# Optimization experiments

Measured on AMD Instinct MI355X. Metric: run time of the kernel, lower is better.

## Reference

```python
import jax, jax.numpy as jnp
import numpy as np

N_HEAD = 12
SEQ = 4096
D_MODEL = 768


def setup_inputs() -> dict:
    key = jax.random.key(0)
    ks = jax.random.split(key, 5)
    tokens = jax.random.normal(ks[0], (SEQ, D_MODEL), dtype=jnp.float32)
    # GPT-2 causal mask buffer: lower-triangular ones, shape [1,1,n_ctx,n_ctx]
    attn_bias = jnp.tril(jnp.ones((SEQ, SEQ), dtype=jnp.float32))[None, None]
    c_attn_weight = jax.random.normal(ks[1], (D_MODEL, 3 * D_MODEL), dtype=jnp.float32) * 0.02
    c_attn_bias = jax.random.normal(ks[2], (3 * D_MODEL,), dtype=jnp.float32) * 0.02
    c_proj_weight = jax.random.normal(ks[3], (D_MODEL, D_MODEL), dtype=jnp.float32) * 0.02
    c_proj_bias = jax.random.normal(ks[4], (D_MODEL,), dtype=jnp.float32) * 0.02
    return {
        "tokens": tokens,
        "attn_bias": attn_bias,
        "c_attn_weight": c_attn_weight,
        "c_attn_bias": c_attn_bias,
        "c_proj_weight": c_proj_weight,
        "c_proj_bias": c_proj_bias,
    }


def reference(tokens, attn_bias, c_attn_weight, c_attn_bias, c_proj_weight, c_proj_bias):
    S, D = tokens.shape
    H = N_HEAD
    hd = D // H
    qkv = tokens @ c_attn_weight + c_attn_bias          # [S, 3D]
    q, k, v = jnp.split(qkv, 3, axis=1)                 # each [S, D]
    q = q.reshape(S, H, hd).transpose(1, 0, 2)          # [H, S, hd]
    kh = k.reshape(S, H, hd).transpose(1, 2, 0)         # [H, hd, S] (key pre-transposed)
    vh = v.reshape(S, H, hd).transpose(1, 0, 2)         # [H, S, hd]
    w = jnp.einsum('hqd,hdk->hqk', q, kh) / jnp.sqrt(jnp.float32(hd))  # [H, S, S]
    nd, ns = S, S
    b = attn_bias[0, :, ns - nd:ns, :ns]                # [1, S, S], broadcasts over heads
    w = w * b - 1e10 * (1.0 - b)
    p = jax.nn.softmax(w, axis=-1)
    a = jnp.einsum('hqk,hkd->hqd', p, vh)               # [H, S, hd]
    a = a.transpose(1, 0, 2).reshape(S, D)              # merge heads
    out = a @ c_proj_weight + c_proj_bias               # [S, D]
    return out
```

## Files before the change

kernel.cpp:

```cpp
#include <hip/hip_runtime.h>

typedef __attribute__((ext_vector_type(8))) short s8v;
typedef __attribute__((ext_vector_type(2))) float f32x2;
typedef __attribute__((ext_vector_type(4))) float f32x4;
typedef __attribute__((ext_vector_type(16))) float f32x16;
typedef __attribute__((ext_vector_type(4))) unsigned short u16x4;
typedef __attribute__((ext_vector_type(4))) unsigned int u32x4;
typedef __attribute__((ext_vector_type(4))) _Float16 h16x4;

#define SEQ 4096
#define DM  768
#define NH  12
#define HD  64
#define QSCL 0.18033688f
#define FOFF 8.0f

__device__ __forceinline__ unsigned short f2bf(float f) {
  union { float f; unsigned int u; } v; v.f = f;
  unsigned int r = v.u + 0x7fffu + ((v.u >> 16) & 1u);
  return (unsigned short)(r >> 16);
}

__device__ __forceinline__ unsigned int cvtpk(float lo, float hi) {
  unsigned int r;
  asm("v_cvt_pk_bf16_f32 %0, %1, %2" : "=v"(r) : "v"(lo), "v"(hi));
  return r;
}

__device__ __forceinline__ void gload16(const void* g, void* l) {
  __builtin_amdgcn_global_load_lds((const __attribute__((address_space(1))) void*)g,
                                   (__attribute__((address_space(3))) void*)l, 16, 0, 0);
}

__global__ __launch_bounds__(256) void k_prep(
    const float* __restrict__ tokens, const float* __restrict__ wqkv,
    const float* __restrict__ wproj, unsigned short* __restrict__ tok,
    unsigned short* __restrict__ wqkvT, unsigned short* __restrict__ wprojT) {
  __shared__ float tile[32][33];
  const int b = blockIdx.x;
  const int tid = threadIdx.x;
  if (b < 3072) {
    int i = (b * 256 + tid) * 4;
    float4 v = *reinterpret_cast<const float4*>(tokens + i);
    u16x4 o;
    o.x = f2bf(v.x); o.y = f2bf(v.y); o.z = f2bf(v.z); o.w = f2bf(v.w);
    *reinterpret_cast<u16x4*>(tok + i) = o;
    return;
  }
  const float* in;
  unsigned short* out;
  int idx, N;
  if (b < 4800) { idx = b - 3072; in = wqkv;  out = wqkvT;  N = 2304; }
  else          { idx = b - 4800; in = wproj; out = wprojT; N = 768;  }
  const int k0 = (idx % 24) * 32, n0 = (idx / 24) * 32;
  const int tr = tid >> 5, tc = tid & 31;
#pragma unroll
  for (int i = 0; i < 4; i++)
    tile[i * 8 + tr][tc] = in[(k0 + i * 8 + tr) * N + n0 + tc];
  __syncthreads();
#pragma unroll
  for (int i = 0; i < 4; i++)
    out[(n0 + i * 8 + tr) * 768 + k0 + tc] = f2bf(tile[tc][i * 8 + tr]);
}

template<int MODE>
__global__ __launch_bounds__(256) void k_gemm(
    const unsigned short* __restrict__ A, const unsigned short* __restrict__ BT,
    const float* __restrict__ bias,
    unsigned short* __restrict__ Oq, unsigned short* __restrict__ Ok,
    unsigned short* __restrict__ Ov, float* __restrict__ Of) {
  __shared__ unsigned short As[128 * 32];
  __shared__ unsigned short Bs[128 * 32];
  const int tid = threadIdx.x;
  const int lane = tid & 63;
  const int w = tid >> 6;
  const int wm = w >> 1, wn = w & 1;
  const int l15 = lane & 15, l4 = lane >> 4;
  const int m0 = blockIdx.x * 128, n0 = blockIdx.y * 128;

  f32x4 acc[4][4] = {};

  int srow[2], skc[2];
#pragma unroll
  for (int j = 0; j < 2; j++) {
    int slot = j * 256 + tid;
    srow[j] = slot >> 2;
    skc[j] = (slot & 3) ^ ((srow[j] >> 1) & 3);
  }
  const int ldsb0 = (tid & ~63) * 16;
  const int ldsb1 = (256 + (tid & ~63)) * 16;

  for (int k0 = 0; k0 < DM; k0 += 32) {
    gload16(A + (m0 + srow[0]) * DM + k0 + skc[0] * 8, (char*)As + ldsb0);
    gload16(A + (m0 + srow[1]) * DM + k0 + skc[1] * 8, (char*)As + ldsb1);
    gload16(BT + (n0 + srow[0]) * DM + k0 + skc[0] * 8, (char*)Bs + ldsb0);
    gload16(BT + (n0 + srow[1]) * DM + k0 + skc[1] * 8, (char*)Bs + ldsb1);
    __syncthreads();
    s8v af[4], bfr[4];
#pragma unroll
    for (int i = 0; i < 4; i++) {
      int ra = wm * 64 + i * 16 + l15;
      int ca = (l4 ^ ((ra >> 1) & 3)) * 8;
      af[i] = *reinterpret_cast<const s8v*>(&As[ra * 32 + ca]);
      int rb = wn * 64 + i * 16 + l15;
      int cb = (l4 ^ ((rb >> 1) & 3)) * 8;
      bfr[i] = *reinterpret_cast<const s8v*>(&Bs[rb * 32 + cb]);
    }
#pragma unroll
    for (int mi = 0; mi < 4; mi++)
#pragma unroll
      for (int nj = 0; nj < 4; nj++)
        acc[mi][nj] = __builtin_amdgcn_mfma_f32_16x16x32_bf16(af[mi], bfr[nj], acc[mi][nj], 0, 0, 0);
    __syncthreads();
  }

#pragma unroll
  for (int nj = 0; nj < 4; nj++) {
    const int col = n0 + wn * 64 + nj * 16 + l15;
    const float bv = bias[col];
#pragma unroll
    for (int mi = 0; mi < 4; mi++) {
      const int rowb = m0 + wm * 64 + mi * 16 + l4 * 4;
      if (MODE == 0) {
        if (col < 768) {
#pragma unroll
          for (int r = 0; r < 4; r++)
            Oq[(rowb + r) * DM + col] = f2bf((acc[mi][nj][r] + bv) * QSCL);
        } else if (col < 1536) {
#pragma unroll
          for (int r = 0; r < 4; r++)
            Ok[(rowb + r) * DM + (col - 768)] = f2bf(acc[mi][nj][r] + bv);
        } else {
          u16x4 pk;
#pragma unroll
          for (int r = 0; r < 4; r++)
            pk[r] = f2bf(acc[mi][nj][r] + bv);
          *reinterpret_cast<u16x4*>(&Ov[(col - 1536) * SEQ + rowb]) = pk;
        }
      } else {
#pragma unroll
        for (int r = 0; r < 4; r++)
          Of[(rowb + r) * DM + col] = acc[mi][nj][r] + bv;
      }
    }
  }
}

__global__ __launch_bounds__(256, 4) void k_attn(
    const unsigned short* __restrict__ Qb, const unsigned short* __restrict__ Kb,
    const unsigned short* __restrict__ Vt, _Float16* __restrict__ Opart,
    float* __restrict__ lw) {
  __shared__ unsigned short Ks[2][64 * 64];
  __shared__ unsigned short Vs[2][64 * 64];
  const int tid = threadIdx.x;
  const int lane = tid & 63;
  const int w = tid >> 6;
  const int l31 = lane & 31, lh = lane >> 5;
  const int bid = blockIdx.x;
  const int s = bid & 3;
  const int b2 = bid >> 2;
  const int head = b2 % NH;
  const int qt = 31 - (b2 / NH);
  const int q0w = qt * 128 + w * 32;
  const int ntiles = 2 * qt + 2;

  const unsigned short* const Kh = Kb + head * HD;
  const unsigned short* const Vh = Vt + head * HD * SEQ;

  int srow[2], scol[2];
#pragma unroll
  for (int j = 0; j < 2; j++) {
    int c = j * 256 + tid;
    srow[j] = c >> 3;
    scol[j] = ((c & 7) ^ (srow[j] & 7)) * 8;
  }
  const int ldsoff0 = (tid & ~63) * 16;
  const int ldsoff1 = 4096 + (tid & ~63) * 16;
  int koff0 = (s * 64 + srow[0]) * DM + scol[0];
  int koff1 = (s * 64 + srow[1]) * DM + scol[1];
  int voff0 = srow[0] * SEQ + s * 64 + scol[0];
  int voff1 = srow[1] * SEQ + s * 64 + scol[1];

  s8v aq[4];
#pragma unroll
  for (int kc = 0; kc < 4; kc++)
    aq[kc] = *reinterpret_cast<const s8v*>(
        &Qb[(q0w + l31) * DM + head * HD + kc * 16 + lh * 8]);

  const int x7 = l31 & 7;
  const int rbase = l31 * 128;

  f32x16 O0 = {}, O1 = {};
  float lsum = 0.f;

  if (s < ntiles) {
    gload16(Kh + koff0, (char*)Ks[0] + ldsoff0);
    gload16(Kh + koff1, (char*)Ks[0] + ldsoff1);
    gload16(Vh + voff0, (char*)Vs[0] + ldsoff0);
    gload16(Vh + voff1, (char*)Vs[0] + ldsoff1);
    __asm__ volatile("s_waitcnt vmcnt(0)" ::: "memory");
  }
  __syncthreads();
  koff0 += 256 * DM; koff1 += 256 * DM;
  voff0 += 256;      voff1 += 256;

  for (int t = s; t < ntiles; t += 4) {
    const int cur = ((t - s) >> 2) & 1;
    if (t + 4 < ntiles) {
      const int nxt = cur ^ 1;
      gload16(Kh + koff0, (char*)Ks[nxt] + ldsoff0);
      gload16(Kh + koff1, (char*)Ks[nxt] + ldsoff1);
      gload16(Vh + voff0, (char*)Vs[nxt] + ldsoff0);
      gload16(Vh + voff1, (char*)Vs[nxt] + ldsoff1);
    }
    koff0 += 256 * DM; koff1 += 256 * DM;
    voff0 += 256;      voff1 += 256;
    const int kb = t * 64;
    if (kb <= q0w + 31) {
      const char* const kbuf = (const char*)Ks[cur];
      const char* const vbuf = (const char*)Vs[cur];
      f32x16 z0, z1;
#pragma unroll
      for (int r = 0; r < 16; r++) { z0[r] = -FOFF; z1[r] = -FOFF; }
      __builtin_amdgcn_s_setprio(1);
#pragma unroll
      for (int kc = 0; kc < 4; kc++) {
        const int so = ((kc * 2 + lh) ^ x7) << 4;
        const s8v k0 = *reinterpret_cast<const s8v*>(kbuf + rbase + so);
        const s8v k1 = *reinterpret_cast<const s8v*>(kbuf + 4096 + rbase + so);
        z0 = __builtin_amdgcn_mfma_f32_32x32x16_bf16(k0, aq[kc], z0, 0, 0, 0);
        z1 = __builtin_amdgcn_mfma_f32_32x32x16_bf16(k1, aq[kc], z1, 0, 0, 0);
      }
      __builtin_amdgcn_s_setprio(0);
      if (kb + 63 > q0w) {
        const int qm = q0w + l31 - kb - 4 * lh;
#pragma unroll
        for (int r = 0; r < 16; r++) {
          const int koff = (r & 3) + 8 * (r >> 2);
          z0[r] = (koff > qm) ? -1e30f : z0[r];
          z1[r] = (koff + 32 > qm) ? -1e30f : z1[r];
        }
      }
      f32x2 sa = {0.f, 0.f}, sb = {0.f, 0.f};
#pragma unroll
      for (int r = 0; r < 8; r++) {
        z0[2 * r] = exp2f(z0[2 * r]);
        z0[2 * r + 1] = exp2f(z0[2 * r + 1]);
        f32x2 e0; e0[0] = z0[2 * r]; e0[1] = z0[2 * r + 1];
        sa += e0;
        z1[2 * r] = exp2f(z1[2 * r]);
        z1[2 * r + 1] = exp2f(z1[2 * r + 1]);
        f32x2 e1; e1[0] = z1[2 * r]; e1[1] = z1[2 * r + 1];
        sb += e1;
      }
      sa += sb;
      lsum += sa[0] + sa[1];
      s8v pf[4];
#define PACKKC(V, base, dst)                                                 \
      {                                                                      \
        unsigned int A0 = cvtpk(V[base + 0], V[base + 1]);                   \
        unsigned int B0 = cvtpk(V[base + 2], V[base + 3]);                   \
        unsigned int A1 = cvtpk(V[base + 4], V[base + 5]);                   \
        unsigned int B1 = cvtpk(V[base + 6], V[base + 7]);                   \
        asm("v_permlane32_swap_b32 %0, %1" : "+v"(A0), "+v"(A1));            \
        asm("v_permlane32_swap_b32 %0, %1" : "+v"(B0), "+v"(B1));            \
        u32x4 q_ = {A0, B0, A1, B1};                                         \
        dst = __builtin_bit_cast(s8v, q_);                                   \
      }
      PACKKC(z0, 0, pf[0]);
      PACKKC(z0, 8, pf[1]);
      PACKKC(z1, 0, pf[2]);
      PACKKC(z1, 8, pf[3]);
#undef PACKKC
      __builtin_amdgcn_s_setprio(1);
#pragma unroll
      for (int kc = 0; kc < 4; kc++) {
        const int so = ((kc * 2 + lh) ^ x7) << 4;
        const s8v v0 = *reinterpret_cast<const s8v*>(vbuf + rbase + so);
        const s8v v1 = *reinterpret_cast<const s8v*>(vbuf + 4096 + rbase + so);
        O0 = __builtin_amdgcn_mfma_f32_32x32x16_bf16(v0, pf[kc], O0, 0, 0, 0);
        O1 = __builtin_amdgcn_mfma_f32_32x32x16_bf16(v1, pf[kc], O1, 0, 0, 0);
      }
      __builtin_amdgcn_s_setprio(0);
    }
    __asm__ volatile("s_waitcnt vmcnt(0)" ::: "memory");
    __syncthreads();
  }

  lsum += __shfl_xor(lsum, 32);
  _Float16* const op = Opart + (size_t)s * SEQ * DM + (size_t)(q0w + l31) * DM +
                       head * HD + 4 * lh;
#pragma unroll
  for (int k = 0; k < 4; k++) {
    h16x4 o0h, o1h;
#pragma unroll
    for (int r = 0; r < 4; r++) {
      o0h[r] = (_Float16)O0[k * 4 + r];
      o1h[r] = (_Float16)O1[k * 4 + r];
    }
    *reinterpret_cast<h16x4*>(op + 8 * k) = o0h;
    *reinterpret_cast<h16x4*>(op + 32 + 8 * k) = o1h;
  }
  if (lh == 0)
    lw[(s * NH + head) * SEQ + q0w + l31] = lsum;
}

__global__ __launch_bounds__(256) void k_merge(const _Float16* __restrict__ Opart,
                                               const float* __restrict__ lw,
                                               unsigned short* __restrict__ attn) {
  const int idx = blockIdx.x * 256 + threadIdx.x;
  const int e4 = idx * 4;
  const int row = e4 / DM;
  const int col = e4 - row * DM;
  const int head = col >> 6;
  const float l0 = lw[(0 * NH + head) * SEQ + row];
  const float l1 = lw[(1 * NH + head) * SEQ + row];
  const float l2 = lw[(2 * NH + head) * SEQ + row];
  const float l3 = lw[(3 * NH + head) * SEQ + row];
  const float rl = 1.f / (l0 + l1 + l2 + l3);
  const size_t SD = (size_t)SEQ * DM;
  const h16x4 o0 = *reinterpret_cast<const h16x4*>(Opart + e4);
  const h16x4 o1 = *reinterpret_cast<const h16x4*>(Opart + SD + e4);
  const h16x4 o2 = *reinterpret_cast<const h16x4*>(Opart + 2 * SD + e4);
  const h16x4 o3 = *reinterpret_cast<const h16x4*>(Opart + 3 * SD + e4);
  u16x4 pk;
#pragma unroll
  for (int j = 0; j < 4; j++)
    pk[j] = f2bf(((float)o0[j] + (float)o1[j] + (float)o2[j] + (float)o3[j]) * rl);
  *reinterpret_cast<u16x4*>(attn + e4) = pk;
}

extern "C" void kernel_launch(void* const* d_in, const int* in_sizes, int n_in,
                              void* d_out, int out_size, void* d_ws, size_t ws_size,
                              hipStream_t stream) {
  (void)in_sizes; (void)n_in; (void)out_size; (void)ws_size;
  const float* tokens = (const float*)d_in[0];
  const float* wqkv  = (const float*)d_in[2];
  const float* bqkv  = (const float*)d_in[3];
  const float* wproj = (const float*)d_in[4];
  const float* bproj = (const float*)d_in[5];
  float* out = (float*)d_out;

  unsigned short* tok    = (unsigned short*)d_ws;
  unsigned short* wqkvT  = tok + 4096 * 768;
  unsigned short* wprojT = wqkvT + 2304 * 768;
  unsigned short* Qb     = wprojT + 768 * 768;
  unsigned short* Kb     = Qb + 4096 * 768;
  unsigned short* Vt     = Kb + 4096 * 768;
  unsigned short* attn   = Vt + 768 * 4096;
  _Float16* Opart = (_Float16*)(attn + 4096 * 768);
  float* lw = (float*)(Opart + 4 * 4096 * 768);

  k_prep<<<5376, 256, 0, stream>>>(tokens, wqkv, wproj, tok, wqkvT, wprojT);
  k_gemm<0><<<dim3(32, 18), 256, 0, stream>>>(tok, wqkvT, bqkv, Qb, Kb, Vt, nullptr);
  k_attn<<<1536, 256, 0, stream>>>(Qb, Kb, Vt, Opart, lw);
  k_merge<<<3072, 256, 0, stream>>>(Opart, lw, attn);
  k_gemm<1><<<dim3(32, 6), 256, 0, stream>>>(attn, wprojT, bproj, nullptr, nullptr, nullptr, out);
}
```

Measured before the change: 103.3 us.

## Double-buffer GEMM LDS tiles and remap blocks across XCDs

```diff
diff --git a/kernel.cpp b/kernel.cpp
--- a/kernel.cpp
+++ b/kernel.cpp
@@ -64,19 +64,21 @@
 }
 
 template<int MODE>
-__global__ __launch_bounds__(256) void k_gemm(
+__global__ __launch_bounds__(256, 4) void k_gemm(
     const unsigned short* __restrict__ A, const unsigned short* __restrict__ BT,
     const float* __restrict__ bias,
     unsigned short* __restrict__ Oq, unsigned short* __restrict__ Ok,
-    unsigned short* __restrict__ Ov, float* __restrict__ Of) {
-  __shared__ unsigned short As[128 * 32];
-  __shared__ unsigned short Bs[128 * 32];
+    unsigned short* __restrict__ Ov, float* __restrict__ Of, int nbx) {
+  __shared__ unsigned short As[2][128 * 32];
+  __shared__ unsigned short Bs[2][128 * 32];
   const int tid = threadIdx.x;
   const int lane = tid & 63;
   const int w = tid >> 6;
   const int wm = w >> 1, wn = w & 1;
   const int l15 = lane & 15, l4 = lane >> 4;
-  const int m0 = blockIdx.x * 128, n0 = blockIdx.y * 128;
+  const int cpx = gridDim.x >> 3;
+  const int wg = (blockIdx.x & 7) * cpx + (blockIdx.x >> 3);
+  const int m0 = (wg % nbx) * 128, n0 = (wg / nbx) * 128;
 
   f32x4 acc[4][4] = {};
 
@@ -89,28 +91,43 @@
   }
   const int ldsb0 = (tid & ~63) * 16;
   const int ldsb1 = (256 + (tid & ~63)) * 16;
+  const int aoff0 = (m0 + srow[0]) * DM + skc[0] * 8;
+  const int aoff1 = (m0 + srow[1]) * DM + skc[1] * 8;
+  const int boff0 = (n0 + srow[0]) * DM + skc[0] * 8;
+  const int boff1 = (n0 + srow[1]) * DM + skc[1] * 8;
+
+  gload16(A + aoff0, (char*)As[0] + ldsb0);
+  gload16(A + aoff1, (char*)As[0] + ldsb1);
+  gload16(BT + boff0, (char*)Bs[0] + ldsb0);
+  gload16(BT + boff1, (char*)Bs[0] + ldsb1);
+  __asm__ volatile("s_waitcnt vmcnt(0)" ::: "memory");
+  __syncthreads();
 
   for (int k0 = 0; k0 < DM; k0 += 32) {
-    gload16(A + (m0 + srow[0]) * DM + k0 + skc[0] * 8, (char*)As + ldsb0);
-    gload16(A + (m0 + srow[1]) * DM + k0 + skc[1] * 8, (char*)As + ldsb1);
-    gload16(BT + (n0 + srow[0]) * DM + k0 + skc[0] * 8, (char*)Bs + ldsb0);
-    gload16(BT + (n0 + srow[1]) * DM + k0 + skc[1] * 8, (char*)Bs + ldsb1);
-    __syncthreads();
+    const int cur = (k0 >> 5) & 1;
+    if (k0 + 32 < DM) {
+      const int nxt = cur ^ 1;
+      gload16(A + aoff0 + k0 + 32, (char*)As[nxt] + ldsb0);
+      gload16(A + aoff1 + k0 + 32, (char*)As[nxt] + ldsb1);
+      gload16(BT + boff0 + k0 + 32, (char*)Bs[nxt] + ldsb0);
+      gload16(BT + boff1 + k0 + 32, (char*)Bs[nxt] + ldsb1);
+    }
     s8v af[4], bfr[4];
 #pragma unroll
     for (int i = 0; i < 4; i++) {
       int ra = wm * 64 + i * 16 + l15;
       int ca = (l4 ^ ((ra >> 1) & 3)) * 8;
-      af[i] = *reinterpret_cast<const s8v*>(&As[ra * 32 + ca]);
+      af[i] = *reinterpret_cast<const s8v*>(&As[cur][ra * 32 + ca]);
       int rb = wn * 64 + i * 16 + l15;
       int cb = (l4 ^ ((rb >> 1) & 3)) * 8;
-      bfr[i] = *reinterpret_cast<const s8v*>(&Bs[rb * 32 + cb]);
+      bfr[i] = *reinterpret_cast<const s8v*>(&Bs[cur][rb * 32 + cb]);
     }
 #pragma unroll
     for (int mi = 0; mi < 4; mi++)
 #pragma unroll
       for (int nj = 0; nj < 4; nj++)
         acc[mi][nj] = __builtin_amdgcn_mfma_f32_16x16x32_bf16(af[mi], bfr[nj], acc[mi][nj], 0, 0, 0);
+    __asm__ volatile("s_waitcnt vmcnt(0)" ::: "memory");
     __syncthreads();
   }
 
@@ -352,8 +369,8 @@
   float* lw = (float*)(Opart + 4 * 4096 * 768);
 
   k_prep<<<5376, 256, 0, stream>>>(tokens, wqkv, wproj, tok, wqkvT, wprojT);
-  k_gemm<0><<<dim3(32, 18), 256, 0, stream>>>(tok, wqkvT, bqkv, Qb, Kb, Vt, nullptr);
+  k_gemm<0><<<576, 256, 0, stream>>>(tok, wqkvT, bqkv, Qb, Kb, Vt, nullptr, 32);
   k_attn<<<1536, 256, 0, stream>>>(Qb, Kb, Vt, Opart, lw);
   k_merge<<<3072, 256, 0, stream>>>(Opart, lw, attn);
-  k_gemm<1><<<dim3(32, 6), 256, 0, stream>>>(attn, wprojT, bproj, nullptr, nullptr, nullptr, out);
-}
+  k_gemm<1><<<192, 256, 0, stream>>>(attn, wprojT, bproj, nullptr, nullptr, nullptr, out, 32);
+}
```

After: 109.5 us. +6.0%, slower.

## Fuse split-KV merge into attention kernel via last-block atomic counter

Applied to the files above, without the earlier changes.

```diff
diff --git a/kernel.cpp b/kernel.cpp
--- a/kernel.cpp
+++ b/kernel.cpp
@@ -149,9 +149,11 @@
 __global__ __launch_bounds__(256, 4) void k_attn(
     const unsigned short* __restrict__ Qb, const unsigned short* __restrict__ Kb,
     const unsigned short* __restrict__ Vt, _Float16* __restrict__ Opart,
-    float* __restrict__ lw) {
+    float* __restrict__ lw, unsigned short* __restrict__ attn,
+    int* __restrict__ cnt) {
   __shared__ unsigned short Ks[2][64 * 64];
   __shared__ unsigned short Vs[2][64 * 64];
+  __shared__ int scnt;
   const int tid = threadIdx.x;
   const int lane = tid & 63;
   const int w = tid >> 6;
@@ -303,31 +305,38 @@
   }
   if (lh == 0)
     lw[(s * NH + head) * SEQ + q0w + l31] = lsum;
-}
-
-__global__ __launch_bounds__(256) void k_merge(const _Float16* __restrict__ Opart,
-                                               const float* __restrict__ lw,
-                                               unsigned short* __restrict__ attn) {
-  const int idx = blockIdx.x * 256 + threadIdx.x;
-  const int e4 = idx * 4;
-  const int row = e4 / DM;
-  const int col = e4 - row * DM;
-  const int head = col >> 6;
-  const float l0 = lw[(0 * NH + head) * SEQ + row];
-  const float l1 = lw[(1 * NH + head) * SEQ + row];
-  const float l2 = lw[(2 * NH + head) * SEQ + row];
-  const float l3 = lw[(3 * NH + head) * SEQ + row];
-  const float rl = 1.f / (l0 + l1 + l2 + l3);
-  const size_t SD = (size_t)SEQ * DM;
-  const h16x4 o0 = *reinterpret_cast<const h16x4*>(Opart + e4);
-  const h16x4 o1 = *reinterpret_cast<const h16x4*>(Opart + SD + e4);
-  const h16x4 o2 = *reinterpret_cast<const h16x4*>(Opart + 2 * SD + e4);
-  const h16x4 o3 = *reinterpret_cast<const h16x4*>(Opart + 3 * SD + e4);
-  u16x4 pk;
-#pragma unroll
-  for (int j = 0; j < 4; j++)
-    pk[j] = f2bf(((float)o0[j] + (float)o1[j] + (float)o2[j] + (float)o3[j]) * rl);
-  *reinterpret_cast<u16x4*>(attn + e4) = pk;
+
+  __syncthreads();
+  if (tid == 0) {
+    __threadfence();
+    scnt = atomicAdd(&cnt[b2], 1);
+  }
+  __syncthreads();
+  if (scnt == 3) {
+    __threadfence();
+    const int row = tid >> 1;
+    const int c0 = (tid & 1) * 32;
+    const int grow = qt * 128 + row;
+    const float l0 = lw[(0 * NH + head) * SEQ + grow];
+    const float l1 = lw[(1 * NH + head) * SEQ + grow];
+    const float l2 = lw[(2 * NH + head) * SEQ + grow];
+    const float l3 = lw[(3 * NH + head) * SEQ + grow];
+    const float rl = 1.f / (l0 + l1 + l2 + l3);
+    const size_t SD = (size_t)SEQ * DM;
+    const size_t base = (size_t)grow * DM + head * HD + c0;
+#pragma unroll
+    for (int c = 0; c < 32; c += 4) {
+      const h16x4 a0 = *reinterpret_cast<const h16x4*>(Opart + base + c);
+      const h16x4 a1 = *reinterpret_cast<const h16x4*>(Opart + SD + base + c);
+      const h16x4 a2 = *reinterpret_cast<const h16x4*>(Opart + 2 * SD + base + c);
+      const h16x4 a3 = *reinterpret_cast<const h16x4*>(Opart + 3 * SD + base + c);
+      u16x4 pk;
+#pragma unroll
+      for (int j = 0; j < 4; j++)
+        pk[j] = f2bf(((float)a0[j] + (float)a1[j] + (float)a2[j] + (float)a3[j]) * rl);
+      *reinterpret_cast<u16x4*>(attn + base + c) = pk;
+    }
+  }
 }
 
 extern "C" void kernel_launch(void* const* d_in, const int* in_sizes, int n_in,
@@ -350,10 +359,11 @@
   unsigned short* attn   = Vt + 768 * 4096;
   _Float16* Opart = (_Float16*)(attn + 4096 * 768);
   float* lw = (float*)(Opart + 4 * 4096 * 768);
-
+  int* cnt = (int*)(lw + 4 * NH * SEQ);
+
+  hipMemsetAsync(cnt, 0, 32 * NH * sizeof(int), stream);
   k_prep<<<5376, 256, 0, stream>>>(tokens, wqkv, wproj, tok, wqkvT, wprojT);
   k_gemm<0><<<dim3(32, 18), 256, 0, stream>>>(tok, wqkvT, bqkv, Qb, Kb, Vt, nullptr);
-  k_attn<<<1536, 256, 0, stream>>>(Qb, Kb, Vt, Opart, lw);
-  k_merge<<<3072, 256, 0, stream>>>(Opart, lw, attn);
+  k_attn<<<1536, 256, 0, stream>>>(Qb, Kb, Vt, Opart, lw, attn, cnt);
   k_gemm<1><<<dim3(32, 6), 256, 0, stream>>>(attn, wprojT, bproj, nullptr, nullptr, nullptr, out);
 }
```

Result: slower. 319.6 us (+209.5%).

## Fuse split-KV merge into output projection GEMM A-tile load

Applied to the files above, without the earlier changes.

```diff
diff --git a/kernel.cpp b/kernel.cpp
--- a/kernel.cpp
+++ b/kernel.cpp
@@ -1,6 +1,7 @@
 #include <hip/hip_runtime.h>
 
 typedef __attribute__((ext_vector_type(8))) short s8v;
+typedef __attribute__((ext_vector_type(8))) _Float16 h16x8;
 typedef __attribute__((ext_vector_type(2))) float f32x2;
 typedef __attribute__((ext_vector_type(4))) float f32x4;
 typedef __attribute__((ext_vector_type(16))) float f32x16;
@@ -49,9 +50,9 @@
   }
   const float* in;
   unsigned short* out;
-  int idx, N;
-  if (b < 4800) { idx = b - 3072; in = wqkv;  out = wqkvT;  N = 2304; }
-  else          { idx = b - 4800; in = wproj; out = wprojT; N = 768;  }
+  int idx, N, asF16;
+  if (b < 4800) { idx = b - 3072; in = wqkv;  out = wqkvT;  N = 2304; asF16 = 0; }
+  else          { idx = b - 4800; in = wproj; out = wprojT; N = 768;  asF16 = 1; }
   const int k0 = (idx % 24) * 32, n0 = (idx / 24) * 32;
   const int tr = tid >> 5, tc = tid & 31;
 #pragma unroll
@@ -59,16 +60,18 @@
     tile[i * 8 + tr][tc] = in[(k0 + i * 8 + tr) * N + n0 + tc];
   __syncthreads();
 #pragma unroll
-  for (int i = 0; i < 4; i++)
-    out[(n0 + i * 8 + tr) * 768 + k0 + tc] = f2bf(tile[tc][i * 8 + tr]);
-}
-
-template<int MODE>
-__global__ __launch_bounds__(256) void k_gemm(
+  for (int i = 0; i < 4; i++) {
+    const float v = tile[tc][i * 8 + tr];
+    out[(n0 + i * 8 + tr) * 768 + k0 + tc] =
+        asF16 ? __builtin_bit_cast(unsigned short, (_Float16)v) : f2bf(v);
+  }
+}
+
+__global__ __launch_bounds__(256) void k_gemm0(
     const unsigned short* __restrict__ A, const unsigned short* __restrict__ BT,
     const float* __restrict__ bias,
     unsigned short* __restrict__ Oq, unsigned short* __restrict__ Ok,
-    unsigned short* __restrict__ Ov, float* __restrict__ Of) {
+    unsigned short* __restrict__ Ov) {
   __shared__ unsigned short As[128 * 32];
   __shared__ unsigned short Bs[128 * 32];
   const int tid = threadIdx.x;
@@ -121,27 +124,107 @@
 #pragma unroll
     for (int mi = 0; mi < 4; mi++) {
       const int rowb = m0 + wm * 64 + mi * 16 + l4 * 4;
-      if (MODE == 0) {
-        if (col < 768) {
-#pragma unroll
-          for (int r = 0; r < 4; r++)
-            Oq[(rowb + r) * DM + col] = f2bf((acc[mi][nj][r] + bv) * QSCL);
-        } else if (col < 1536) {
-#pragma unroll
-          for (int r = 0; r < 4; r++)
-            Ok[(rowb + r) * DM + (col - 768)] = f2bf(acc[mi][nj][r] + bv);
-        } else {
-          u16x4 pk;
-#pragma unroll
-          for (int r = 0; r < 4; r++)
-            pk[r] = f2bf(acc[mi][nj][r] + bv);
-          *reinterpret_cast<u16x4*>(&Ov[(col - 1536) * SEQ + rowb]) = pk;
-        }
+      if (col < 768) {
+#pragma unroll
+        for (int r = 0; r < 4; r++)
+          Oq[(rowb + r) * DM + col] = f2bf((acc[mi][nj][r] + bv) * QSCL);
+      } else if (col < 1536) {
+#pragma unroll
+        for (int r = 0; r < 4; r++)
+          Ok[(rowb + r) * DM + (col - 768)] = f2bf(acc[mi][nj][r] + bv);
       } else {
+        u16x4 pk;
 #pragma unroll
         for (int r = 0; r < 4; r++)
-          Of[(rowb + r) * DM + col] = acc[mi][nj][r] + bv;
-      }
+          pk[r] = f2bf(acc[mi][nj][r] + bv);
+        *reinterpret_cast<u16x4*>(&Ov[(col - 1536) * SEQ + rowb]) = pk;
+      }
+    }
+  }
+}
+
+__global__ __launch_bounds__(256) void k_gemm2(
+    const _Float16* __restrict__ Opart, const float* __restrict__ lw,
+    const _Float16* __restrict__ BT, const float* __restrict__ bias,
+    float* __restrict__ Of) {
+  __shared__ _Float16 As[128 * 32];
+  __shared__ _Float16 Bs[128 * 32];
+  __shared__ float rlt[128][12];
+  const int tid = threadIdx.x;
+  const int lane = tid & 63;
+  const int w = tid >> 6;
+  const int wm = w >> 1, wn = w & 1;
+  const int l15 = lane & 15, l4 = lane >> 4;
+  const int m0 = blockIdx.x * 128, n0 = blockIdx.y * 128;
+  const size_t SD = (size_t)SEQ * DM;
+
+  for (int e = tid; e < 128 * 12; e += 256) {
+    const int r = e / 12, h = e - r * 12;
+    const int grow = m0 + r;
+    const float l = lw[(0 * NH + h) * SEQ + grow] + lw[(1 * NH + h) * SEQ + grow] +
+                    lw[(2 * NH + h) * SEQ + grow] + lw[(3 * NH + h) * SEQ + grow];
+    rlt[r][h] = 1.f / l;
+  }
+
+  f32x4 acc[4][4] = {};
+
+  int srow[2], skc[2];
+#pragma unroll
+  for (int j = 0; j < 2; j++) {
+    int slot = j * 256 + tid;
+    srow[j] = slot >> 2;
+    skc[j] = (slot & 3) ^ ((srow[j] >> 1) & 3);
+  }
+  const int ldsb0 = (tid & ~63) * 16;
+  const int ldsb1 = (256 + (tid & ~63)) * 16;
+  const size_t aoff[2] = {(size_t)(m0 + srow[0]) * DM + skc[0] * 8,
+                          (size_t)(m0 + srow[1]) * DM + skc[1] * 8};
+  h16x8* const awr[2] = {reinterpret_cast<h16x8*>((char*)As + (size_t)tid * 16),
+                         reinterpret_cast<h16x8*>((char*)As + (size_t)(256 + tid) * 16)};
+  __syncthreads();
+
+  for (int k0 = 0; k0 < DM; k0 += 32) {
+#pragma unroll
+    for (int j = 0; j < 2; j++) {
+      const size_t base = aoff[j] + k0;
+      const h16x8 a0 = *reinterpret_cast<const h16x8*>(Opart + base);
+      const h16x8 a1 = *reinterpret_cast<const h16x8*>(Opart + SD + base);
+      const h16x8 a2 = *reinterpret_cast<const h16x8*>(Opart + 2 * SD + base);
+      const h16x8 a3 = *reinterpret_cast<const h16x8*>(Opart + 3 * SD + base);
+      const _Float16 rl = (_Float16)rlt[srow[j]][(k0 + skc[j] * 8) >> 6];
+      *awr[j] = ((a0 + a1) + (a2 + a3)) * rl;
+    }
+    gload16(BT + (n0 + srow[0]) * DM + k0 + skc[0] * 8, (char*)Bs + ldsb0);
+    gload16(BT + (n0 + srow[1]) * DM + k0 + skc[1] * 8, (char*)Bs + ldsb1);
+    __syncthreads();
+    h16x8 af[4], bfr[4];
+#pragma unroll
+    for (int i = 0; i < 4; i++) {
+      int ra = wm * 64 + i * 16 + l15;
+      int ca = (l4 ^ ((ra >> 1) & 3)) * 8;
+      af[i] = *reinterpret_cast<const h16x8*>(&As[ra * 32 + ca]);
+      int rb = wn * 64 + i * 16 + l15;
+      int cb = (l4 ^ ((rb >> 1) & 3)) * 8;
+      bfr[i] = *reinterpret_cast<const h16x8*>(&Bs[rb * 32 + cb]);
+    }
+#pragma unroll
+    for (int mi = 0; mi < 4; mi++)
+#pragma unroll
+      for (int nj = 0; nj < 4; nj++)
+        acc[mi][nj] = __builtin_amdgcn_mfma_f32_16x16x32_f16(af[mi], bfr[nj], acc[mi][nj], 0, 0, 0);
+    __syncthreads();
+  }
+
+#pragma unroll
+  for (int nj = 0; nj < 4; nj++) {
+    const int col = n0 + wn * 64 + nj * 16 + l15;
+    const float bv = bias[col];
+#pragma unroll
+    for (int mi = 0; mi < 4; mi++) {
+      const int rowb = m0 + wm * 64 + mi * 16 + l4 * 4;
+#pragma unroll
+      for (int r = 0; r < 4; r++)
+        Of[(rowb + r) * DM + col] = acc[mi][nj][r] + bv;
     }
   }
 }
@@ -305,31 +388,6 @@
     lw[(s * NH + head) * SEQ + q0w + l31] = lsum;
 }
 
-__global__ __launch_bounds__(256) void k_merge(const _Float16* __restrict__ Opart,
-                                               const float* __restrict__ lw,
-                                               unsigned short* __restrict__ attn) {
-  const int idx = blockIdx.x * 256 + threadIdx.x;
-  const int e4 = idx * 4;
-  const int row = e4 / DM;
-  const int col = e4 - row * DM;
-  const int head = col >> 6;
-  const float l0 = lw[(0 * NH + head) * SEQ + row];
-  const float l1 = lw[(1 * NH + head) * SEQ + row];
-  const float l2 = lw[(2 * NH + head) * SEQ + row];
-  const float l3 = lw[(3 * NH + head) * SEQ + row];
-  const float rl = 1.f / (l0 + l1 + l2 + l3);
-  const size_t SD = (size_t)SEQ * DM;
-  const h16x4 o0 = *reinterpret_cast<const h16x4*>(Opart + e4);
-  const h16x4 o1 = *reinterpret_cast<const h16x4*>(Opart + SD + e4);
-  const h16x4 o2 = *reinterpret_cast<const h16x4*>(Opart + 2 * SD + e4);
-  const h16x4 o3 = *reinterpret_cast<const h16x4*>(Opart + 3 * SD + e4);
-  u16x4 pk;
-#pragma unroll
-  for (int j = 0; j < 4; j++)
-    pk[j] = f2bf(((float)o0[j] + (float)o1[j] + (float)o2[j] + (float)o3[j]) * rl);
-  *reinterpret_cast<u16x4*>(attn + e4) = pk;
-}
-
 extern "C" void kernel_launch(void* const* d_in, const int* in_sizes, int n_in,
                               void* d_out, int out_size, void* d_ws, size_t ws_size,
                               hipStream_t stream) {
@@ -349,11 +407,11 @@
   unsigned short* Vt     = Kb + 4096 * 768;
   unsigned short* attn   = Vt + 768 * 4096;
   _Float16* Opart = (_Float16*)(attn + 4096 * 768);
-  float* lw = (float*)(Opart + 4 * 4096 * 768);
+  float* lw = (float*)(Opart + 4 * (size_t)4096 * 768);
 
   k_prep<<<5376, 256, 0, stream>>>(tokens, wqkv, wproj, tok, wqkvT, wprojT);
-  k_gemm<0><<<dim3(32, 18), 256, 0, stream>>>(tok, wqkvT, bqkv, Qb, Kb, Vt, nullptr);
+  k_gemm0<<<dim3(32, 18), 256, 0, stream>>>(tok, wqkvT, bqkv, Qb, Kb, Vt);
   k_attn<<<1536, 256, 0, stream>>>(Qb, Kb, Vt, Opart, lw);
-  k_merge<<<3072, 256, 0, stream>>>(Opart, lw, attn);
-  k_gemm<1><<<dim3(32, 6), 256, 0, stream>>>(attn, wprojT, bproj, nullptr, nullptr, nullptr, out);
-}
+  k_gemm2<<<dim3(32, 6), 256, 0, stream>>>(Opart, lw, (const _Float16*)wprojT,
+                                           bproj, out);
+}
```

Result: slower. 115.3 us (+11.6%).
